# Kernel optimization log

Hardware: AMD Instinct MI355X
Metric: run time of the kernel (lower is better)

Reference implementation:

```python
import jax, jax.numpy as jnp
import numpy as np

N_NODES = 10000
N_EDGES = 80000
A, C, D = 2, 15, 64     # batch, temporal dim (15 fixed by fc conv kernel), feature dim
OUT_DIM = 10            # fixed by fc conv kernel width
N_GIN = 2               # num_layers - 1 GIN conv layers
BN_EPS = 1e-5


def bn_last(x, g, b):
    # torch BatchNorm2d (training-mode batch stats) with channels on the LAST axis;
    # original code permutes (0,3,2,1) around BN, which is equivalent to normalizing axis -1.
    m = x.mean(axis=(0, 1, 2), keepdims=True)
    v = x.var(axis=(0, 1, 2), keepdims=True)  # biased var, as torch uses in forward
    return (x - m) * jax.lax.rsqrt(v + BN_EPS) * g + b


def setup_inputs() -> dict:
    key = jax.random.key(0)
    ks = jax.random.split(key, 16)
    s = 0.05
    f32 = jnp.float32
    return {
        "h": jax.random.normal(ks[0], (A, D, C, N_NODES), f32),
        # GIN layer params, stacked over the 2 layers (input_dim == hidden_dim == 64)
        "eps": jnp.zeros((N_GIN,), f32),                                   # learn_eps, init 0
        "W0": (jax.random.normal(ks[1], (N_GIN, D, D), f32) * s),          # MLP linear 0
        "b0": jnp.zeros((N_GIN, D), f32),
        "g0": jnp.ones((N_GIN, D), f32),                                   # MLP BN
        "be0": jnp.zeros((N_GIN, D), f32),
        "W1": (jax.random.normal(ks[2], (N_GIN, D, D), f32) * s),          # MLP linear 1
        "b1": jnp.zeros((N_GIN, D), f32),
        "ga": jnp.ones((N_GIN, D), f32),                                   # ApplyNodeFunc BN
        "ba": jnp.zeros((N_GIN, D), f32),
        "go": jnp.ones((N_GIN, D), f32),                                   # outer GIN BN
        "bo": jnp.zeros((N_GIN, D), f32),
        # per-hidden-rep prediction linears (3 = num_layers)
        "Wp": (jax.random.normal(ks[3], (N_GIN + 1, D, OUT_DIM), f32) * s),
        "bp": jnp.zeros((N_GIN + 1, OUT_DIM), f32),
        # final Conv2d(1,1,(15,10)) == full-extent weighted sum
        "Wfc": (jax.random.normal(ks[4], (C, OUT_DIM), f32) * s),
        "bfc": jnp.zeros((1,), f32),
        # graph edge list (src -> dst aggregation)
        "src": jax.random.randint(ks[5], (N_EDGES,), 0, N_NODES, jnp.int32),
        "dst": jax.random.randint(ks[6], (N_EDGES,), 0, N_NODES, jnp.int32),
    }


def reference(h, eps, W0, b0, g0, be0, W1, b1, ga, ba, go, bo, Wp, bp, Wfc, bfc, src, dst):
    # h: [A, D, C, N] -> node-first layout [N, A, C, D] (the two transposes in torch)
    x = jnp.transpose(h, (3, 0, 2, 1))
    hidden_rep = [x]
    for l in range(N_GIN):
        # GINConv, sum aggregation: (1+eps)*h + sum_{src->dst} h[src]
        agg = jax.ops.segment_sum(x[src], dst, num_segments=N_NODES)
        z = (1.0 + eps[l]) * x + agg
        # MLP (2 layers): linear -> BN -> relu -> linear
        z = jax.nn.relu(bn_last(z @ W0[l] + b0[l], g0[l], be0[l]))
        z = z @ W1[l] + b1[l]
        # ApplyNodeFunc: BN + relu
        z = jax.nn.relu(bn_last(z, ga[l], ba[l]))
        # outer per-layer BN + relu (GIN.forward)
        x = jax.nn.relu(bn_last(z, go[l], bo[l]))
        hidden_rep.append(x)
    # multi-scale readout: sum-pool over nodes, per-layer linear score (dropout is eval/no-op)
    score = jnp.zeros((A, C, OUT_DIM), h.dtype)
    for i, r in enumerate(hidden_rep):
        pooled = r.sum(axis=0)                       # [A, C, D]
        score = score + pooled @ Wp[i] + bp[i]
    # fc: Conv2d(1,1,(15,10)) over [A,1,C,OUT_DIM] then squeeze twice -> [A, 1]
    out = jnp.einsum('ach,ch->a', score, Wfc) + bfc[0]
    return out[:, None]
```

## Files before the change

### kernel.cpp

```cpp
#include <hip/hip_runtime.h>
#include <hip/hip_bf16.h>

#define N_NODES   10000
#define N_EDGES   80000
#define R_TOTAL   300000
#define ELEMS     19200000
#define NODE_F    1920
#define N_TILES   18750
#define PD_GRID   640
#define GEMM_GRID 1024
#define RP_BGRP   16

typedef __attribute__((ext_vector_type(8))) short short8;
typedef __attribute__((ext_vector_type(4))) float f32x4;
typedef __attribute__((ext_vector_type(4))) unsigned int u32x4;
typedef __attribute__((ext_vector_type(2))) unsigned int u32x2;
typedef unsigned short ushort_t;

__device__ __forceinline__ unsigned short f2bf(float f) {
    unsigned u = __builtin_bit_cast(unsigned, f);
    unsigned r = u + 0x7fff + ((u >> 16) & 1);
    return (unsigned short)(r >> 16);
}
__device__ __forceinline__ float lo_f(unsigned u) { return __builtin_bit_cast(float, u << 16); }
__device__ __forceinline__ float hi_f(unsigned u) { return __builtin_bit_cast(float, u & 0xffff0000u); }
__device__ __forceinline__ unsigned packbf(float lo, float hi) {
    return ((unsigned)f2bf(hi) << 16) | (unsigned)f2bf(lo);
}

__device__ __forceinline__ void bn_coef(const float* __restrict__ ssum,
                                        const float* __restrict__ ssq,
                                        const float* __restrict__ g,
                                        const float* __restrict__ b, int j,
                                        float& sc, float& sh) {
    const float invM = 1.0f / (float)R_TOTAL;
    float m = ssum[j] * invM;
    float v = ssq[j] * invM - m * m;
    sc = g[j] * rsqrtf(v + 1e-5f);
    sh = b[j] - m * sc;
}

__global__ __launch_bounds__(256) void k_transpose(const float* __restrict__ h,
                                                   ushort_t* __restrict__ xb,
                                                   float* __restrict__ pooled) {
    __shared__ float tile[64][65];
    int tn = blockIdx.x;
    int ac = blockIdx.y;
    int a = ac / 15, c = ac % 15;
    int t = threadIdx.x;
    int n0 = tn * 64;

    int r = t >> 4, g = t & 15;
    int nbase = n0 + 4 * g;
    const float* hp = h + (size_t)a * 9600000 + (size_t)c * 10000;
#pragma unroll
    for (int it = 0; it < 4; it++) {
        int d = it * 16 + r;
        const float* p = hp + (size_t)d * 150000 + nbase;
        float4 v;
        if (nbase + 3 < N_NODES) {
            v = *(const float4*)p;
        } else {
            v.x = (nbase + 0 < N_NODES) ? p[0] : 0.f;
            v.y = (nbase + 1 < N_NODES) ? p[1] : 0.f;
            v.z = (nbase + 2 < N_NODES) ? p[2] : 0.f;
            v.w = (nbase + 3 < N_NODES) ? p[3] : 0.f;
        }
        tile[d][4 * g + 0] = v.x;
        tile[d][4 * g + 1] = v.y;
        tile[d][4 * g + 2] = v.z;
        tile[d][4 * g + 3] = v.w;
    }
    __syncthreads();

    int nn = t >> 2, dg = (t & 3) * 16;
    int n = n0 + nn;
    if (n < N_NODES) {
        u32x4 oA, oB;
#pragma unroll
        for (int q = 0; q < 4; q++) {
            oA[q] = packbf(tile[dg + 2 * q][nn],     tile[dg + 2 * q + 1][nn]);
            oB[q] = packbf(tile[dg + 8 + 2 * q][nn], tile[dg + 8 + 2 * q + 1][nn]);
        }
        ushort_t* dst = xb + ((size_t)(n * 30 + ac)) * 64 + dg;
        *(u32x4*)dst = oA;
        *(u32x4*)(dst + 8) = oB;
    }

    if (t < 64) {
        float s = 0.f;
        int lim = min(64, N_NODES - n0);
        for (int j = 0; j < lim; j++) s += tile[t][j];
        atomicAdd(&pooled[ac * 64 + t], s);
    }
}

__global__ void k_deg(const int* __restrict__ dst, int* __restrict__ deg) {
    int e = blockIdx.x * 256 + threadIdx.x;
    if (e < N_EDGES) atomicAdd(&deg[dst[e]], 1);
}

__global__ __launch_bounds__(256) void k_scan(const int* __restrict__ deg,
                                              int* __restrict__ off,
                                              int* __restrict__ cursor) {
    __shared__ int buf[256];
    int t = threadIdx.x;
    int c0 = t * 40;
    int local[40];
    int s = 0;
    for (int i = 0; i < 40; i++) {
        int idx = c0 + i;
        int d = (idx < N_NODES) ? deg[idx] : 0;
        local[i] = d;
        s += d;
    }
    buf[t] = s;
    __syncthreads();
    for (int st = 1; st < 256; st <<= 1) {
        int v = (t >= st) ? buf[t - st] : 0;
        __syncthreads();
        buf[t] += v;
        __syncthreads();
    }
    int run = buf[t] - s;
    for (int i = 0; i < 40; i++) {
        int idx = c0 + i;
        if (idx < N_NODES) {
            off[idx] = run;
            cursor[idx] = run;
            run += local[i];
        }
    }
    if (t == 255) off[N_NODES] = buf[255];
}

__global__ void k_fill(const int* __restrict__ src, const int* __restrict__ dst,
                       int* __restrict__ cursor, int* __restrict__ csr) {
    int e = blockIdx.x * 256 + threadIdx.x;
    if (e < N_EDGES) {
        int p = atomicAdd(&cursor[dst[e]], 1);
        csr[p] = src[e];
    }
}

__global__ __launch_bounds__(256) void k_gather(const ushort_t* __restrict__ xb,
                                                ushort_t* __restrict__ aggb,
                                                const int* __restrict__ off,
                                                const int* __restrict__ csr) {
    __shared__ int eds[256];
    int n = blockIdx.x;
    int t = threadIdx.x;
    bool act = t < 240;
    int e0 = off[n], e1 = off[n + 1];
    float acc[8] = {0.f, 0.f, 0.f, 0.f, 0.f, 0.f, 0.f, 0.f};
    for (int base = e0; base < e1; base += 256) {
        int cnt = min(256, e1 - base);
        __syncthreads();
        if (t < cnt) eds[t] = csr[base + t];
        __syncthreads();
        if (act) {
            int i = 0;
            for (; i + 8 <= cnt; i += 8) {
                u32x4 v0 = *(const u32x4*)(xb + (size_t)eds[i + 0] * NODE_F + t * 8);
                u32x4 v1 = *(const u32x4*)(xb + (size_t)eds[i + 1] * NODE_F + t * 8);
                u32x4 v2 = *(const u32x4*)(xb + (size_t)eds[i + 2] * NODE_F + t * 8);
                u32x4 v3 = *(const u32x4*)(xb + (size_t)eds[i + 3] * NODE_F + t * 8);
                u32x4 v4 = *(const u32x4*)(xb + (size_t)eds[i + 4] * NODE_F + t * 8);
                u32x4 v5 = *(const u32x4*)(xb + (size_t)eds[i + 5] * NODE_F + t * 8);
                u32x4 v6 = *(const u32x4*)(xb + (size_t)eds[i + 6] * NODE_F + t * 8);
                u32x4 v7 = *(const u32x4*)(xb + (size_t)eds[i + 7] * NODE_F + t * 8);
#pragma unroll
                for (int q = 0; q < 4; q++) {
                    acc[2 * q]     += (lo_f(v0[q]) + lo_f(v1[q])) + (lo_f(v2[q]) + lo_f(v3[q]))
                                    + (lo_f(v4[q]) + lo_f(v5[q])) + (lo_f(v6[q]) + lo_f(v7[q]));
                    acc[2 * q + 1] += (hi_f(v0[q]) + hi_f(v1[q])) + (hi_f(v2[q]) + hi_f(v3[q]))
                                    + (hi_f(v4[q]) + hi_f(v5[q])) + (hi_f(v6[q]) + hi_f(v7[q]));
                }
            }
            for (; i + 4 <= cnt; i += 4) {
                u32x4 v0 = *(const u32x4*)(xb + (size_t)eds[i + 0] * NODE_F + t * 8);
                u32x4 v1 = *(const u32x4*)(xb + (size_t)eds[i + 1] * NODE_F + t * 8);
                u32x4 v2 = *(const u32x4*)(xb + (size_t)eds[i + 2] * NODE_F + t * 8);
                u32x4 v3 = *(const u32x4*)(xb + (size_t)eds[i + 3] * NODE_F + t * 8);
#pragma unroll
                for (int q = 0; q < 4; q++) {
                    acc[2 * q]     += (lo_f(v0[q]) + lo_f(v1[q])) + (lo_f(v2[q]) + lo_f(v3[q]));
                    acc[2 * q + 1] += (hi_f(v0[q]) + hi_f(v1[q])) + (hi_f(v2[q]) + hi_f(v3[q]));
                }
            }
            for (; i < cnt; i++) {
                u32x4 v = *(const u32x4*)(xb + (size_t)eds[i] * NODE_F + t * 8);
#pragma unroll
                for (int q = 0; q < 4; q++) {
                    acc[2 * q]     += lo_f(v[q]);
                    acc[2 * q + 1] += hi_f(v[q]);
                }
            }
        }
    }
    if (act) {
        u32x4 o;
#pragma unroll
        for (int q = 0; q < 4; q++) o[q] = packbf(acc[2 * q], acc[2 * q + 1]);
        *(u32x4*)(aggb + (size_t)n * NODE_F + t * 8) = o;
    }
}

__global__ __launch_bounds__(256) void k_passA(const ushort_t* __restrict__ xb,
                                               const ushort_t* __restrict__ aggb,
                                               ushort_t* __restrict__ to,
                                               const float* __restrict__ W,
                                               const float* __restrict__ bias,
                                               const float* __restrict__ epsp, int l,
                                               float* __restrict__ ssum, float* __restrict__ ssq) {
    int tid = threadIdx.x;
    int lane = tid & 63, wid = tid >> 6;
    int m = lane & 15, kg = lane >> 4;

    short8 bfr[2][4];
#pragma unroll
    for (int s = 0; s < 2; s++)
#pragma unroll
        for (int nt = 0; nt < 4; nt++) {
            short8 v;
#pragma unroll
            for (int j = 0; j < 8; j++)
                v[j] = (short)f2bf(W[(s * 32 + kg * 8 + j) * 64 + 4 * m + nt]);
            bfr[s][nt] = v;
        }
    float bcol[4];
#pragma unroll
    for (int nt = 0; nt < 4; nt++) bcol[nt] = bias[4 * m + nt];
    float e1 = 1.0f + epsp[l];

    float s0a[4] = {0.f, 0.f, 0.f, 0.f}, s1a[4] = {0.f, 0.f, 0.f, 0.f};

    for (int tile = blockIdx.x * 4 + wid; tile < N_TILES; tile += gridDim.x * 4) {
        size_t row0 = (size_t)tile * 16;
        const u32x4* xr = (const u32x4*)(xb + (row0 + m) * 64);
        const u32x4* ar = (const u32x4*)(aggb + (row0 + m) * 64);
        short8 afr[2];
#pragma unroll
        for (int s = 0; s < 2; s++) {
            u32x4 xv = xr[s * 4 + kg];
            u32x4 av = ar[s * 4 + kg];
            u32x4 zv;
#pragma unroll
            for (int q = 0; q < 4; q++) {
                float zl = fmaf(e1, lo_f(xv[q]), lo_f(av[q]));
                float zh = fmaf(e1, hi_f(xv[q]), hi_f(av[q]));
                zv[q] = packbf(zl, zh);
            }
            afr[s] = __builtin_bit_cast(short8, zv);
        }
        f32x4 acc0 = {0,0,0,0}, acc1 = {0,0,0,0}, acc2 = {0,0,0,0}, acc3 = {0,0,0,0};
#pragma unroll
        for (int s = 0; s < 2; s++) {
            acc0 = __builtin_amdgcn_mfma_f32_16x16x32_bf16(afr[s], bfr[s][0], acc0, 0, 0, 0);
            acc1 = __builtin_amdgcn_mfma_f32_16x16x32_bf16(afr[s], bfr[s][1], acc1, 0, 0, 0);
            acc2 = __builtin_amdgcn_mfma_f32_16x16x32_bf16(afr[s], bfr[s][2], acc2, 0, 0, 0);
            acc3 = __builtin_amdgcn_mfma_f32_16x16x32_bf16(afr[s], bfr[s][3], acc3, 0, 0, 0);
        }
        ushort_t* tw = to + (row0 + kg * 4) * 64 + 4 * m;
#pragma unroll
        for (int r = 0; r < 4; r++) {
            float v0 = acc0[r] + bcol[0];
            float v1 = acc1[r] + bcol[1];
            float v2 = acc2[r] + bcol[2];
            float v3 = acc3[r] + bcol[3];
            u32x2 pk;
            pk[0] = packbf(v0, v1);
            pk[1] = packbf(v2, v3);
            *(u32x2*)(tw + (size_t)r * 64) = pk;
            s0a[0] += v0; s1a[0] += v0 * v0;
            s0a[1] += v1; s1a[1] += v1 * v1;
            s0a[2] += v2; s1a[2] += v2 * v2;
            s0a[3] += v3; s1a[3] += v3 * v3;
        }
    }
    __shared__ float shs0[64], shs1[64];
    if (tid < 64) { shs0[tid] = 0.f; shs1[tid] = 0.f; }
    __syncthreads();
#pragma unroll
    for (int nt = 0; nt < 4; nt++) {
        atomicAdd(&shs0[4 * m + nt], s0a[nt]);
        atomicAdd(&shs1[4 * m + nt], s1a[nt]);
    }
    __syncthreads();
    if (tid < 64) {
        atomicAdd(&ssum[tid], shs0[tid]);
        atomicAdd(&ssq[tid], shs1[tid]);
    }
}

__global__ __launch_bounds__(256) void k_passB(const ushort_t* __restrict__ ti,
                                               ushort_t* __restrict__ to,
                                               const float* __restrict__ W,
                                               const float* __restrict__ bias,
                                               const float* __restrict__ ssum0,
                                               const float* __restrict__ ssq0,
                                               const float* __restrict__ g0,
                                               const float* __restrict__ be0,
                                               float* __restrict__ ssum, float* __restrict__ ssq) {
    int tid = threadIdx.x;
    int lane = tid & 63, wid = tid >> 6;
    int m = lane & 15, kg = lane >> 4;

    short8 bfr[2][4];
#pragma unroll
    for (int s = 0; s < 2; s++)
#pragma unroll
        for (int nt = 0; nt < 4; nt++) {
            short8 v;
#pragma unroll
            for (int j = 0; j < 8; j++)
                v[j] = (short)f2bf(W[(s * 32 + kg * 8 + j) * 64 + 4 * m + nt]);
            bfr[s][nt] = v;
        }
    float bcol[4];
#pragma unroll
    for (int nt = 0; nt < 4; nt++) bcol[nt] = bias[4 * m + nt];
    float scv[2][8], shv[2][8];
#pragma unroll
    for (int s = 0; s < 2; s++)
#pragma unroll
        for (int j = 0; j < 8; j++)
            bn_coef(ssum0, ssq0, g0, be0, s * 32 + kg * 8 + j, scv[s][j], shv[s][j]);

    float s0a[4] = {0.f, 0.f, 0.f, 0.f}, s1a[4] = {0.f, 0.f, 0.f, 0.f};

    for (int tile = blockIdx.x * 4 + wid; tile < N_TILES; tile += gridDim.x * 4) {
        size_t row0 = (size_t)tile * 16;
        const u32x4* tr = (const u32x4*)(ti + (row0 + m) * 64);
        short8 afr[2];
#pragma unroll
        for (int s = 0; s < 2; s++) {
            u32x4 tv = tr[s * 4 + kg];
            u32x4 zv;
#pragma unroll
            for (int q = 0; q < 4; q++) {
                float zl_ = fmaxf(fmaf(lo_f(tv[q]), scv[s][2 * q],     shv[s][2 * q]),     0.f);
                float zh_ = fmaxf(fmaf(hi_f(tv[q]), scv[s][2 * q + 1], shv[s][2 * q + 1]), 0.f);
                zv[q] = packbf(zl_, zh_);
            }
            afr[s] = __builtin_bit_cast(short8, zv);
        }
        f32x4 acc0 = {0,0,0,0}, acc1 = {0,0,0,0}, acc2 = {0,0,0,0}, acc3 = {0,0,0,0};
#pragma unroll
        for (int s = 0; s < 2; s++) {
            acc0 = __builtin_amdgcn_mfma_f32_16x16x32_bf16(afr[s], bfr[s][0], acc0, 0, 0, 0);
            acc1 = __builtin_amdgcn_mfma_f32_16x16x32_bf16(afr[s], bfr[s][1], acc1, 0, 0, 0);
            acc2 = __builtin_amdgcn_mfma_f32_16x16x32_bf16(afr[s], bfr[s][2], acc2, 0, 0, 0);
            acc3 = __builtin_amdgcn_mfma_f32_16x16x32_bf16(afr[s], bfr[s][3], acc3, 0, 0, 0);
        }
        ushort_t* tw = to + (row0 + kg * 4) * 64 + 4 * m;
#pragma unroll
        for (int r = 0; r < 4; r++) {
            float v0 = acc0[r] + bcol[0];
            float v1 = acc1[r] + bcol[1];
            float v2 = acc2[r] + bcol[2];
            float v3 = acc3[r] + bcol[3];
            u32x2 pk;
            pk[0] = packbf(v0, v1);
            pk[1] = packbf(v2, v3);
            *(u32x2*)(tw + (size_t)r * 64) = pk;
            s0a[0] += v0; s1a[0] += v0 * v0;
            s0a[1] += v1; s1a[1] += v1 * v1;
            s0a[2] += v2; s1a[2] += v2 * v2;
            s0a[3] += v3; s1a[3] += v3 * v3;
        }
    }
    __shared__ float shs0[64], shs1[64];
    if (tid < 64) { shs0[tid] = 0.f; shs1[tid] = 0.f; }
    __syncthreads();
#pragma unroll
    for (int nt = 0; nt < 4; nt++) {
        atomicAdd(&shs0[4 * m + nt], s0a[nt]);
        atomicAdd(&shs1[4 * m + nt], s1a[nt]);
    }
    __syncthreads();
    if (tid < 64) {
        atomicAdd(&ssum[tid], shs0[tid]);
        atomicAdd(&ssq[tid], shs1[tid]);
    }
}

__global__ __launch_bounds__(256) void k_statsC(const ushort_t* __restrict__ tb,
                                                const float* __restrict__ ssum1,
                                                const float* __restrict__ ssq1,
                                                const float* __restrict__ ga,
                                                const float* __restrict__ ba,
                                                float* __restrict__ ssum2,
                                                float* __restrict__ ssq2) {
    __shared__ float shs0[64], shs1[64];
    int tid = threadIdx.x;
    if (tid < 64) { shs0[tid] = 0.f; shs1[tid] = 0.f; }
    __syncthreads();
    int ch0 = (tid & 7) * 8;
    float sc[8], sh[8];
#pragma unroll
    for (int j = 0; j < 8; j++) bn_coef(ssum1, ssq1, ga, ba, ch0 + j, sc[j], sh[j]);
    float s0[8] = {0,0,0,0,0,0,0,0}, s1[8] = {0,0,0,0,0,0,0,0};
    const u32x4* t4 = (const u32x4*)tb;
    const int total = ELEMS / 8;
    int stride = gridDim.x * 256;
    for (int i = blockIdx.x * 256 + tid; i < total; i += stride) {
        u32x4 v = t4[i];
#pragma unroll
        for (int q = 0; q < 4; q++) {
            float e;
            e = fmaxf(fmaf(lo_f(v[q]), sc[2 * q],     sh[2 * q]),     0.f);
            s0[2 * q] += e;     s1[2 * q] += e * e;
            e = fmaxf(fmaf(hi_f(v[q]), sc[2 * q + 1], sh[2 * q + 1]), 0.f);
            s0[2 * q + 1] += e; s1[2 * q + 1] += e * e;
        }
    }
#pragma unroll
    for (int j = 0; j < 8; j++) {
        atomicAdd(&shs0[ch0 + j], s0[j]);
        atomicAdd(&shs1[ch0 + j], s1[j]);
    }
    __syncthreads();
    if (tid < 64) {
        atomicAdd(&ssum2[tid], shs0[tid]);
        atomicAdd(&ssq2[tid], shs1[tid]);
    }
}

__global__ __launch_bounds__(256) void k_passD(const ushort_t* __restrict__ tb,
                                               ushort_t* __restrict__ xb,
                                               const float* __restrict__ ssum1,
                                               const float* __restrict__ ssq1,
                                               const float* __restrict__ ga,
                                               const float* __restrict__ ba,
                                               const float* __restrict__ ssum2,
                                               const float* __restrict__ ssq2,
                                               const float* __restrict__ go,
                                               const float* __restrict__ bo,
                                               float* __restrict__ pp,
                                               int writeX) {
    int t = threadIdx.x;
    bool act = t < 240;
    int ch0 = (t & 7) * 8;
    float sc1[8], sh1[8], sc2[8], sh2[8];
#pragma unroll
    for (int j = 0; j < 8; j++) {
        bn_coef(ssum1, ssq1, ga, ba, ch0 + j, sc1[j], sh1[j]);
        bn_coef(ssum2, ssq2, go, bo, ch0 + j, sc2[j], sh2[j]);
    }
    float pool[8] = {0,0,0,0,0,0,0,0};
    if (act) {
        for (int n = blockIdx.x; n < N_NODES; n += gridDim.x) {
            const u32x4* tr = (const u32x4*)(tb + (size_t)n * NODE_F);
            u32x4 v = tr[t];
            u32x4 o;
#pragma unroll
            for (int q = 0; q < 4; q++) {
                float el = fmaxf(fmaf(fmaxf(fmaf(lo_f(v[q]), sc1[2 * q], sh1[2 * q]), 0.f),
                                      sc2[2 * q], sh2[2 * q]), 0.f);
                float eh = fmaxf(fmaf(fmaxf(fmaf(hi_f(v[q]), sc1[2 * q + 1], sh1[2 * q + 1]), 0.f),
                                      sc2[2 * q + 1], sh2[2 * q + 1]), 0.f);
                pool[2 * q] += el;
                pool[2 * q + 1] += eh;
                o[q] = packbf(el, eh);
            }
            if (writeX) *(u32x4*)(xb + (size_t)n * NODE_F + t * 8) = o;
        }
        float4* pb = (float4*)(pp + (size_t)blockIdx.x * NODE_F + t * 8);
        pb[0] = make_float4(pool[0], pool[1], pool[2], pool[3]);
        pb[1] = make_float4(pool[4], pool[5], pool[6], pool[7]);
    }
}

__global__ __launch_bounds__(256) void k_redpool(const float* __restrict__ pp0,
                                                 const float* __restrict__ pp1,
                                                 float* __restrict__ pooled) {
    int ch = blockIdx.x * 256 + threadIdx.x;
    if (ch >= NODE_F) return;
    const float* pp = (blockIdx.z == 0) ? pp0 : pp1;
    float* dstp = pooled + (blockIdx.z + 1) * NODE_F;
    const int per = PD_GRID / RP_BGRP;
    int b0 = blockIdx.y * per;
    float a0 = 0.f, a1 = 0.f, a2 = 0.f, a3 = 0.f;
    for (int b = b0; b < b0 + per; b += 4) {
        a0 += pp[(size_t)(b + 0) * NODE_F + ch];
        a1 += pp[(size_t)(b + 1) * NODE_F + ch];
        a2 += pp[(size_t)(b + 2) * NODE_F + ch];
        a3 += pp[(size_t)(b + 3) * NODE_F + ch];
    }
    atomicAdd(&dstp[ch], (a0 + a1) + (a2 + a3));
}

__global__ void k_final(const float* __restrict__ pooled,
                        const float* __restrict__ Wp,
                        const float* __restrict__ bp,
                        const float* __restrict__ Wfc,
                        const float* __restrict__ bfc, float* __restrict__ out) {
    __shared__ float oa[2];
    int t = threadIdx.x;
    if (t < 2) oa[t] = 0.f;
    __syncthreads();
    if (t < 300) {
        int a = t / 150, rem = t % 150, c = rem / 10, hh = rem % 10;
        int ac = a * 15 + c;
        float sc_sum = 0.f;
        for (int i = 0; i < 3; i++) {
            float s = bp[i * 10 + hh];
            const float* pp = pooled + i * NODE_F + ac * 64;
            const float* wp = Wp + i * 640 + hh;
            for (int d = 0; d < 64; d++) s += pp[d] * wp[d * 10];
            sc_sum += s;
        }
        atomicAdd(&oa[a], sc_sum * Wfc[c * 10 + hh]);
    }
    __syncthreads();
    if (t < 2) out[t] = oa[t] + bfc[0];
}

extern "C" void kernel_launch(void* const* d_in, const int* in_sizes, int n_in,
                              void* d_out, int out_size, void* d_ws, size_t ws_size,
                              hipStream_t stream) {
    const float* h   = (const float*)d_in[0];
    const float* eps = (const float*)d_in[1];
    const float* W0  = (const float*)d_in[2];
    const float* b0  = (const float*)d_in[3];
    const float* g0  = (const float*)d_in[4];
    const float* be0 = (const float*)d_in[5];
    const float* W1  = (const float*)d_in[6];
    const float* b1  = (const float*)d_in[7];
    const float* ga  = (const float*)d_in[8];
    const float* ba  = (const float*)d_in[9];
    const float* go  = (const float*)d_in[10];
    const float* bo  = (const float*)d_in[11];
    const float* Wp  = (const float*)d_in[12];
    const float* bp  = (const float*)d_in[13];
    const float* Wfc = (const float*)d_in[14];
    const float* bfc = (const float*)d_in[15];
    const int*   src = (const int*)d_in[16];
    const int*   dst = (const int*)d_in[17];
    float* out = (float*)d_out;

    ushort_t* xb   = (ushort_t*)d_ws;
    ushort_t* bufP = xb + ELEMS;
    ushort_t* bufQ = bufP + ELEMS;
    float* small   = (float*)(bufQ + ELEMS);
    float* bn = small;
    float* pooled = small + 6 * 256;
    int* ideg = (int*)(pooled + 3 * NODE_F);
    int* ioff = ideg + N_NODES;
    int* icur = ioff + N_NODES + 1;
    int* icsr = icur + N_NODES;
    float* pp0 = (float*)(icsr + N_EDGES);
    float* pp1 = pp0 + (size_t)PD_GRID * NODE_F;

    hipMemsetAsync(small, 0,
                   (6 * 256 + 3 * NODE_F) * sizeof(float) + N_NODES * sizeof(int), stream);

    k_deg<<<(N_EDGES + 255) / 256, 256, 0, stream>>>(dst, ideg);
    k_scan<<<1, 256, 0, stream>>>(ideg, ioff, icur);
    k_fill<<<(N_EDGES + 255) / 256, 256, 0, stream>>>(src, dst, icur, icsr);

    k_transpose<<<dim3(157, 30), 256, 0, stream>>>(h, xb, pooled);

    for (int l = 0; l < 2; l++) {
        float* s0s = bn + l * 3 * 256;
        float* s1s = s0s + 256;
        float* s2s = s1s + 256;
        float* ppl = (l == 0) ? pp0 : pp1;
        k_gather<<<N_NODES, 256, 0, stream>>>(xb, bufP, ioff, icsr);
        k_passA<<<GEMM_GRID, 256, 0, stream>>>(xb, bufP, bufQ,
                                               W0 + l * 4096, b0 + l * 64, eps, l,
                                               s0s, s0s + 64);
        k_passB<<<GEMM_GRID, 256, 0, stream>>>(bufQ, bufP, W1 + l * 4096, b1 + l * 64,
                                               s0s, s0s + 64, g0 + l * 64, be0 + l * 64,
                                               s1s, s1s + 64);
        k_statsC<<<1024, 256, 0, stream>>>(bufP, s1s, s1s + 64, ga + l * 64, ba + l * 64,
                                           s2s, s2s + 64);
        k_passD<<<PD_GRID, 256, 0, stream>>>(bufP, xb, s1s, s1s + 64, ga + l * 64, ba + l * 64,
                                             s2s, s2s + 64, go + l * 64, bo + l * 64,
                                             ppl, (l == 0) ? 1 : 0);
    }
    k_redpool<<<dim3(8, RP_BGRP, 2), 256, 0, stream>>>(pp0, pp1, pooled);
    k_final<<<1, 320, 0, stream>>>(pooled, Wp, bp, Wfc, bfc, out);
}
```

Measured before the change: 447.5 us.

## Fuse second MLP linear, BN stats and final BN passes into cooperative kernel

Replaces the separate passB, statsC and passD kernels with one cooperative kernel. Each block keeps its 25 tiles of the second-linear output in shared memory and uses grid-wide syncs between the BN-statistics phases, so the intermediate no longer round-trips through global memory. The pooling partials are reused from a workspace buffer and reduced per layer. This removes two kernel launches and the global writes and reads of the intermediate per layer, but needs all 750 blocks co-resident. That depends on large shared-memory use and a 3-blocks-per-SM launch bound, and the code falls back to the old kernels if the cooperative launch fails.

```diff
diff --git a/kernel.cpp b/kernel.cpp
--- a/kernel.cpp
+++ b/kernel.cpp
@@ -1,5 +1,8 @@
 #include <hip/hip_runtime.h>
 #include <hip/hip_bf16.h>
+#include <hip/hip_cooperative_groups.h>
+
+namespace cg = cooperative_groups;
 
 #define N_NODES   10000
 #define N_EDGES   80000
@@ -9,7 +12,8 @@
 #define N_TILES   18750
 #define PD_GRID   640
 #define GEMM_GRID 1024
-#define RP_BGRP   16
+#define FB_GRID   750
+#define FT_TILES  25
 
 typedef __attribute__((ext_vector_type(8))) short short8;
 typedef __attribute__((ext_vector_type(4))) float f32x4;
@@ -26,6 +30,10 @@
 __device__ __forceinline__ float hi_f(unsigned u) { return __builtin_bit_cast(float, u & 0xffff0000u); }
 __device__ __forceinline__ unsigned packbf(float lo, float hi) {
     return ((unsigned)f2bf(hi) << 16) | (unsigned)f2bf(lo);
+}
+
+__device__ __forceinline__ float coh_load(const float* p) {
+    return __hip_atomic_load(p, __ATOMIC_RELAXED, __HIP_MEMORY_SCOPE_AGENT);
 }
 
 __device__ __forceinline__ void bn_coef(const float* __restrict__ ssum,
@@ -36,6 +44,18 @@
     const float invM = 1.0f / (float)R_TOTAL;
     float m = ssum[j] * invM;
     float v = ssq[j] * invM - m * m;
+    sc = g[j] * rsqrtf(v + 1e-5f);
+    sh = b[j] - m * sc;
+}
+
+__device__ __forceinline__ void bn_coef_coh(const float* __restrict__ ssum,
+                                            const float* __restrict__ ssq,
+                                            const float* __restrict__ g,
+                                            const float* __restrict__ b, int j,
+                                            float& sc, float& sh) {
+    const float invM = 1.0f / (float)R_TOTAL;
+    float m = coh_load(&ssum[j]) * invM;
+    float v = coh_load(&ssq[j]) * invM - m * m;
     sc = g[j] * rsqrtf(v + 1e-5f);
     sh = b[j] - m * sc;
 }
@@ -293,6 +313,175 @@
     }
 }
 
+__global__ __launch_bounds__(256, 3) void k_fusedBCD(
+        const ushort_t* __restrict__ t1buf,
+        ushort_t* __restrict__ xb,
+        const float* __restrict__ W,
+        const float* __restrict__ bias,
+        const float* __restrict__ ssum0, const float* __restrict__ ssq0,
+        const float* __restrict__ g0, const float* __restrict__ be0,
+        float* __restrict__ ssum1, float* __restrict__ ssq1,
+        const float* __restrict__ ga, const float* __restrict__ ba,
+        float* __restrict__ ssum2, float* __restrict__ ssq2,
+        const float* __restrict__ go, const float* __restrict__ bo,
+        float* __restrict__ pp, int writeX) {
+    __shared__ ushort_t t3l[FT_TILES * 1024];
+    __shared__ float shs0[64], shs1[64];
+    cg::grid_group grid = cg::this_grid();
+
+    int t = threadIdx.x;
+    int lane = t & 63, w = t >> 6;
+    int m = lane & 15, kg = lane >> 4;
+    int bid = blockIdx.x;
+    int t0 = bid * FT_TILES;
+    int c8 = t & 7;
+
+    float sc_a[8], sh_a[8];
+
+    {
+        short8 bfr[2][4];
+#pragma unroll
+        for (int s = 0; s < 2; s++)
+#pragma unroll
+            for (int ntc = 0; ntc < 4; ntc++) {
+                short8 v;
+#pragma unroll
+                for (int j = 0; j < 8; j++)
+                    v[j] = (short)f2bf(W[(s * 32 + kg * 8 + j) * 64 + 4 * m + ntc]);
+                bfr[s][ntc] = v;
+            }
+        float bcol[4];
+#pragma unroll
+        for (int ntc = 0; ntc < 4; ntc++) bcol[ntc] = bias[4 * m + ntc];
+        float scv[2][8], shv[2][8];
+#pragma unroll
+        for (int s = 0; s < 2; s++)
+#pragma unroll
+            for (int j = 0; j < 8; j++)
+                bn_coef(ssum0, ssq0, g0, be0, s * 32 + kg * 8 + j, scv[s][j], shv[s][j]);
+
+        if (t < 64) { shs0[t] = 0.f; shs1[t] = 0.f; }
+        __syncthreads();
+
+        float s0a[4] = {0.f, 0.f, 0.f, 0.f}, s1a[4] = {0.f, 0.f, 0.f, 0.f};
+        for (int ti = w; ti < FT_TILES; ti += 4) {
+            size_t row0 = (size_t)(t0 + ti) * 16;
+            const u32x4* tr = (const u32x4*)(t1buf + (row0 + m) * 64);
+            short8 afr[2];
+#pragma unroll
+            for (int s = 0; s < 2; s++) {
+                u32x4 tv = tr[s * 4 + kg];
+                u32x4 zv;
+#pragma unroll
+                for (int q = 0; q < 4; q++) {
+                    float zl_ = fmaxf(fmaf(lo_f(tv[q]), scv[s][2 * q],     shv[s][2 * q]),     0.f);
+                    float zh_ = fmaxf(fmaf(hi_f(tv[q]), scv[s][2 * q + 1], shv[s][2 * q + 1]), 0.f);
+                    zv[q] = packbf(zl_, zh_);
+                }
+                afr[s] = __builtin_bit_cast(short8, zv);
+            }
+            f32x4 acc0 = {0,0,0,0}, acc1 = {0,0,0,0}, acc2 = {0,0,0,0}, acc3 = {0,0,0,0};
+#pragma unroll
+            for (int s = 0; s < 2; s++) {
+                acc0 = __builtin_amdgcn_mfma_f32_16x16x32_bf16(afr[s], bfr[s][0], acc0, 0, 0, 0);
+                acc1 = __builtin_amdgcn_mfma_f32_16x16x32_bf16(afr[s], bfr[s][1], acc1, 0, 0, 0);
+                acc2 = __builtin_amdgcn_mfma_f32_16x16x32_bf16(afr[s], bfr[s][2], acc2, 0, 0, 0);
+                acc3 = __builtin_amdgcn_mfma_f32_16x16x32_bf16(afr[s], bfr[s][3], acc3, 0, 0, 0);
+            }
+            ushort_t* tw = t3l + ((size_t)ti * 16 + kg * 4) * 64 + 4 * m;
+#pragma unroll
+            for (int r = 0; r < 4; r++) {
+                float v0 = acc0[r] + bcol[0];
+                float v1 = acc1[r] + bcol[1];
+                float v2 = acc2[r] + bcol[2];
+                float v3 = acc3[r] + bcol[3];
+                u32x2 pk;
+                pk[0] = packbf(v0, v1);
+                pk[1] = packbf(v2, v3);
+                *(u32x2*)(tw + (size_t)r * 64) = pk;
+                s0a[0] += v0; s1a[0] += v0 * v0;
+                s0a[1] += v1; s1a[1] += v1 * v1;
+                s0a[2] += v2; s1a[2] += v2 * v2;
+                s0a[3] += v3; s1a[3] += v3 * v3;
+            }
+        }
+#pragma unroll
+        for (int ntc = 0; ntc < 4; ntc++) {
+            atomicAdd(&shs0[4 * m + ntc], s0a[ntc]);
+            atomicAdd(&shs1[4 * m + ntc], s1a[ntc]);
+        }
+        __syncthreads();
+        if (t < 64) {
+            atomicAdd(&ssum1[t], shs0[t]);
+            atomicAdd(&ssq1[t], shs1[t]);
+        }
+    }
+    grid.sync();
+
+#pragma unroll
+    for (int j = 0; j < 8; j++)
+        bn_coef_coh(ssum1, ssq1, ga, ba, c8 * 8 + j, sc_a[j], sh_a[j]);
+    {
+        if (t < 64) { shs0[t] = 0.f; shs1[t] = 0.f; }
+        __syncthreads();
+        float s0[8] = {0,0,0,0,0,0,0,0}, s1[8] = {0,0,0,0,0,0,0,0};
+        const int nchunks = FT_TILES * 128;
+        for (int idx = t; idx < nchunks; idx += 256) {
+            u32x4 v = *(const u32x4*)(t3l + (size_t)idx * 8);
+#pragma unroll
+            for (int q = 0; q < 4; q++) {
+                float e;
+                e = fmaxf(fmaf(lo_f(v[q]), sc_a[2 * q],     sh_a[2 * q]),     0.f);
+                s0[2 * q] += e;     s1[2 * q] += e * e;
+                e = fmaxf(fmaf(hi_f(v[q]), sc_a[2 * q + 1], sh_a[2 * q + 1]), 0.f);
+                s0[2 * q + 1] += e; s1[2 * q + 1] += e * e;
+            }
+        }
+#pragma unroll
+        for (int j = 0; j < 8; j++) {
+            atomicAdd(&shs0[c8 * 8 + j], s0[j]);
+            atomicAdd(&shs1[c8 * 8 + j], s1[j]);
+        }
+        __syncthreads();
+        if (t < 64) {
+            atomicAdd(&ssum2[t], shs0[t]);
+            atomicAdd(&ssq2[t], shs1[t]);
+        }
+    }
+    grid.sync();
+
+    if (t < 240) {
+        int ac = t >> 3;
+        float sc_o[8], sh_o[8];
+#pragma unroll
+        for (int j = 0; j < 8; j++)
+            bn_coef_coh(ssum2, ssq2, go, bo, c8 * 8 + j, sc_o[j], sh_o[j]);
+        float pool[8] = {0,0,0,0,0,0,0,0};
+        int r0 = t0 * 16;
+        int rend = r0 + FT_TILES * 16;
+        int rfirst = r0 + ((ac - (r0 % 30)) % 30 + 30) % 30;
+        for (int r = rfirst; r < rend; r += 30) {
+            int lr = r - r0;
+            u32x4 v = *(const u32x4*)(t3l + (size_t)lr * 64 + c8 * 8);
+            u32x4 o;
+#pragma unroll
+            for (int q = 0; q < 4; q++) {
+                float ul = fmaxf(fmaf(lo_f(v[q]), sc_a[2 * q],     sh_a[2 * q]),     0.f);
+                float uh = fmaxf(fmaf(hi_f(v[q]), sc_a[2 * q + 1], sh_a[2 * q + 1]), 0.f);
+                float yl = fmaxf(fmaf(ul, sc_o[2 * q],     sh_o[2 * q]),     0.f);
+                float yh = fmaxf(fmaf(uh, sc_o[2 * q + 1], sh_o[2 * q + 1]), 0.f);
+                pool[2 * q] += yl;
+                pool[2 * q + 1] += yh;
+                o[q] = packbf(yl, yh);
+            }
+            if (writeX) *(u32x4*)(xb + (size_t)r * 64 + c8 * 8) = o;
+        }
+        float4* pb = (float4*)(pp + (size_t)bid * NODE_F + ac * 64 + c8 * 8);
+        pb[0] = make_float4(pool[0], pool[1], pool[2], pool[3]);
+        pb[1] = make_float4(pool[4], pool[5], pool[6], pool[7]);
+    }
+}
+
 __global__ __launch_bounds__(256) void k_passB(const ushort_t* __restrict__ ti,
                                                ushort_t* __restrict__ to,
                                                const float* __restrict__ W,
@@ -472,23 +661,14 @@
     }
 }
 
-__global__ __launch_bounds__(256) void k_redpool(const float* __restrict__ pp0,
-                                                 const float* __restrict__ pp1,
-                                                 float* __restrict__ pooled) {
+__global__ __launch_bounds__(256) void k_redpool(const float* __restrict__ pp,
+                                                 float* __restrict__ dstp, int nrows) {
     int ch = blockIdx.x * 256 + threadIdx.x;
     if (ch >= NODE_F) return;
-    const float* pp = (blockIdx.z == 0) ? pp0 : pp1;
-    float* dstp = pooled + (blockIdx.z + 1) * NODE_F;
-    const int per = PD_GRID / RP_BGRP;
-    int b0 = blockIdx.y * per;
-    float a0 = 0.f, a1 = 0.f, a2 = 0.f, a3 = 0.f;
-    for (int b = b0; b < b0 + per; b += 4) {
-        a0 += pp[(size_t)(b + 0) * NODE_F + ch];
-        a1 += pp[(size_t)(b + 1) * NODE_F + ch];
-        a2 += pp[(size_t)(b + 2) * NODE_F + ch];
-        a3 += pp[(size_t)(b + 3) * NODE_F + ch];
-    }
-    atomicAdd(&dstp[ch], (a0 + a1) + (a2 + a3));
+    float a = 0.f;
+    for (int b = blockIdx.y; b < nrows; b += 16)
+        a += pp[(size_t)b * NODE_F + ch];
+    atomicAdd(&dstp[ch], a);
 }
 
 __global__ void k_final(const float* __restrict__ pooled,
@@ -550,8 +730,7 @@
     int* ioff = ideg + N_NODES;
     int* icur = ioff + N_NODES + 1;
     int* icsr = icur + N_NODES;
-    float* pp0 = (float*)(icsr + N_EDGES);
-    float* pp1 = pp0 + (size_t)PD_GRID * NODE_F;
+    float* pp_l = (float*)bufQ;
 
     hipMemsetAsync(small, 0,
                    (6 * 256 + 3 * NODE_F) * sizeof(float) + N_NODES * sizeof(int), stream);
@@ -566,20 +745,46 @@
         float* s0s = bn + l * 3 * 256;
         float* s1s = s0s + 256;
         float* s2s = s1s + 256;
-        float* ppl = (l == 0) ? pp0 : pp1;
         k_gather<<<N_NODES, 256, 0, stream>>>(xb, bufP, ioff, icsr);
         k_passA<<<GEMM_GRID, 256, 0, stream>>>(xb, bufP, bufQ,
                                                W0 + l * 4096, b0 + l * 64, eps, l,
                                                s0s, s0s + 64);
-        k_passB<<<GEMM_GRID, 256, 0, stream>>>(bufQ, bufP, W1 + l * 4096, b1 + l * 64,
-                                               s0s, s0s + 64, g0 + l * 64, be0 + l * 64,
-                                               s1s, s1s + 64);
-        k_statsC<<<1024, 256, 0, stream>>>(bufP, s1s, s1s + 64, ga + l * 64, ba + l * 64,
-                                           s2s, s2s + 64);
-        k_passD<<<PD_GRID, 256, 0, stream>>>(bufP, xb, s1s, s1s + 64, ga + l * 64, ba + l * 64,
-                                             s2s, s2s + 64, go + l * 64, bo + l * 64,
-                                             ppl, (l == 0) ? 1 : 0);
-    }
-    k_redpool<<<dim3(8, RP_BGRP, 2), 256, 0, stream>>>(pp0, pp1, pooled);
+        int nrows;
+        {
+            const ushort_t* t1p = bufQ;
+            ushort_t* xbp = xb;
+            const float* Wp1 = W1 + l * 4096;
+            const float* bp1 = b1 + l * 64;
+            const float* ss0 = s0s;         const float* sq0 = s0s + 64;
+            const float* g0p = g0 + l * 64; const float* be0p = be0 + l * 64;
+            float* ss1 = s1s;               float* sq1 = s1s + 64;
+            const float* gap = ga + l * 64; const float* bap = ba + l * 64;
+            float* ss2 = s2s;               float* sq2 = s2s + 64;
+            const float* gop = go + l * 64; const float* bop = bo + l * 64;
+            float* ppl = pp_l;
+            int wx = (l == 0) ? 1 : 0;
+            void* args[] = {
+                (void*)&t1p, (void*)&xbp, (void*)&Wp1, (void*)&bp1,
+                (void*)&ss0, (void*)&sq0, (void*)&g0p, (void*)&be0p,
+                (void*)&ss1, (void*)&sq1, (void*)&gap, (void*)&bap,
+                (void*)&ss2, (void*)&sq2, (void*)&gop, (void*)&bop,
+                (void*)&ppl, (void*)&wx
+            };
+            hipError_t ce = hipLaunchCooperativeKernel((const void*)k_fusedBCD,
+                                                       dim3(FB_GRID), dim3(256),
+                                                       args, 0, stream);
+            if (ce == hipSuccess) {
+                nrows = FB_GRID;
+            } else {
+                k_passB<<<GEMM_GRID, 256, 0, stream>>>(bufQ, bufP, Wp1, bp1,
+                                                       ss0, sq0, g0p, be0p, ss1, sq1);
+                k_statsC<<<1024, 256, 0, stream>>>(bufP, ss1, sq1, gap, bap, ss2, sq2);
+                k_passD<<<PD_GRID, 256, 0, stream>>>(bufP, xb, ss1, sq1, gap, bap,
+                                                     ss2, sq2, gop, bop, pp_l, wx);
+                nrows = PD_GRID;
+            }
+        }
+        k_redpool<<<dim3(8, 16), 256, 0, stream>>>(pp_l, pooled + (l + 1) * NODE_F, nrows);
+    }
     k_final<<<1, 320, 0, stream>>>(pooled, Wp, bp, Wfc, bfc, out);
 }
```

Measured after the change: 648.9 us. 45.0% more time.
